# Kernel optimization log

Measured on AMD Instinct MI355X. Metric: run time of the kernel, lower is better.

The kernel has to match this reference:

```python
import jax, jax.numpy as jnp
import numpy as np

N_NODES = 50000
N_EDGES = 800000
N_GRAPHS = 64
D = 96              # input_dim = hidden_dim = output_dim
N_GIN = 4           # num_layers - 1 GINConv layers
N_HEADS = 5         # num_layers linear_prediction heads
BN_EPS = 1e-5


def setup_inputs() -> dict:
    key = jax.random.key(0)
    ks = jax.random.split(key, 16)
    s = 1.0 / np.sqrt(D)
    h = jax.random.normal(ks[0], (N_NODES, D), dtype=jnp.float32)
    src = jax.random.randint(ks[1], (N_EDGES,), 0, N_NODES, dtype=jnp.int32)
    dst = jax.random.randint(ks[2], (N_EDGES,), 0, N_NODES, dtype=jnp.int32)
    # sorted node->graph ids; deterministic so every graph is non-empty
    graph_ids = (jnp.arange(N_NODES, dtype=jnp.int32) * N_GRAPHS) // N_NODES
    return {
        "h": h,
        # GIN layer MLPs (num_mlp_layers=2): Linear -> BN -> ReLU -> Linear
        "gin_W1": jax.random.uniform(ks[3], (N_GIN, D, D), jnp.float32, -s, s),
        "gin_b1": jax.random.uniform(ks[4], (N_GIN, D), jnp.float32, -s, s),
        "gin_bn1_g": jnp.ones((N_GIN, D), jnp.float32),
        "gin_bn1_b": jnp.zeros((N_GIN, D), jnp.float32),
        "gin_W2": jax.random.uniform(ks[5], (N_GIN, D, D), jnp.float32, -s, s),
        "gin_b2": jax.random.uniform(ks[6], (N_GIN, D), jnp.float32, -s, s),
        # per-layer outer BatchNorm1d
        "bn_g": jnp.ones((N_GIN, D), jnp.float32),
        "bn_b": jnp.zeros((N_GIN, D), jnp.float32),
        # shared PReLU parameter (nn.PReLU default: 1 param, init 0.25)
        "prelu_a": jnp.full((1,), 0.25, jnp.float32),
        # linear_prediction heads
        "lin_W": jax.random.uniform(ks[7], (N_HEADS, D, D), jnp.float32, -s, s),
        "lin_b": jax.random.uniform(ks[8], (N_HEADS, D), jnp.float32, -s, s),
        "src": src,
        "dst": dst,
        "graph_ids": graph_ids,
    }


def _batchnorm(x, gamma, beta):
    # training-mode batch statistics over the node dim (biased variance, as torch)
    m = jnp.mean(x, axis=0)
    v = jnp.var(x, axis=0)
    return gamma * (x - m) * jax.lax.rsqrt(v + BN_EPS) + beta


def reference(h, gin_W1, gin_b1, gin_bn1_g, gin_bn1_b, gin_W2, gin_b2,
              bn_g, bn_b, prelu_a, lin_W, lin_b, src, dst, graph_ids):
    hidden_rep = [h]
    for l in range(N_GIN):
        # GINConv, sum aggregation, eps=0 (learn_eps=False): (1+eps)*h + sum_{j in N(i)} h_j
        agg = jax.ops.segment_sum(h[src], dst, num_segments=N_NODES)  # [N, D]
        z = h + agg
        # apply_func MLP: Linear -> BN -> ReLU -> Linear
        z = jax.nn.relu(_batchnorm(z @ gin_W1[l] + gin_b1[l], gin_bn1_g[l], gin_bn1_b[l]))
        z = z @ gin_W2[l] + gin_b2[l]
        # outer BatchNorm + PReLU
        z = _batchnorm(z, bn_g[l], bn_b[l])
        h = jnp.where(z >= 0, z, prelu_a * z)
        hidden_rep.append(h)
    # max graph pooling + per-layer linear heads (dropout = identity in eval)
    reps = []
    for l, hr in enumerate(hidden_rep):
        pooled = jax.ops.segment_max(hr, graph_ids, num_segments=N_GRAPHS)  # [B, D]
        reps.append(pooled @ lin_W[l] + lin_b[l])
    # layer_aggregation='cat': stack on dim=-1 then flatten -> [B, D * (N_GIN+1)]
    return jnp.stack(reps, axis=-1).reshape(N_GRAPHS, -1)
```

## Files before the change

kernel.cpp:

```cpp
#include <hip/hip_runtime.h>
#include <hip/hip_bf16.h>

#define N_NODES 50000
#define N_EDGES 800000
#define N_GRAPHS 64
#define D 96
#define N_GIN 4
#define BN_EPS 1e-5f
#define PCH 64
#define GEMM_GRID 782
#define LP 104
#define ELLCAP 64

#define P1_BLOCKS 256
#define EPB 3125
#define BSH 8
#define BNODES 256
#define NBUCK 196
#define SPITCH 33

typedef __bf16 bf16;
typedef __bf16 bf16x8 __attribute__((ext_vector_type(8)));
typedef float f32x4 __attribute__((ext_vector_type(4)));
typedef unsigned short u16;
typedef unsigned int u32;

__device__ inline unsigned enc(float f) {
    unsigned b = __float_as_uint(f);
    return (b & 0x80000000u) ? ~b : (b | 0x80000000u);
}
__device__ inline float dec(unsigned u) {
    return __uint_as_float((u & 0x80000000u) ? (u ^ 0x80000000u) : ~u);
}

__global__ void k_prolog(const float* __restrict__ h, bf16* __restrict__ hb,
                         const float* __restrict__ W1, const float* __restrict__ W2,
                         bf16* __restrict__ wf, float* __restrict__ stats,
                         unsigned* __restrict__ pooledu) {
    int b = blockIdx.x;
    int tid = threadIdx.x;
    if (b < 2344) {
        int e = (b * 256 + tid) * 8;
        if (e >= N_NODES * D) return;
        float4 v0 = *(const float4*)(h + e);
        float4 v1 = *(const float4*)(h + e + 4);
        bf16x8 o;
        o[0] = (bf16)v0.x; o[1] = (bf16)v0.y; o[2] = (bf16)v0.z; o[3] = (bf16)v0.w;
        o[4] = (bf16)v1.x; o[5] = (bf16)v1.y; o[6] = (bf16)v1.z; o[7] = (bf16)v1.w;
        *(bf16x8*)(hb + e) = o;
    } else if (b < 2352) {
        int mat = b - 2344;
        const float* src = (mat < 4) ? (W1 + mat * D * D) : (W2 + (mat - 4) * D * D);
        bf16* dst = wf + mat * D * D;
        for (int p = tid; p < D * D; p += 256) {
            int f = p >> 9;
            int r = p & 511;
            int lane = r >> 3;
            int j = r & 7;
            int q = lane >> 4;
            int m16 = lane & 15;
            int nt = f / 3, ks = f % 3;
            int k = ks * 32 + q * 8 + j;
            int n = nt * 16 + m16;
            dst[p] = (bf16)src[k * D + n];
        }
    } else {
        int t = (b - 2352) * 256 + tid;
        if (t < N_GIN * 2 * 2 * D) stats[t] = 0.0f;
        if (t < 5 * N_GRAPHS * D) pooledu[t] = 0u;
    }
}

__global__ void __launch_bounds__(256) k_part_pool(
        const int* __restrict__ src, const int* __restrict__ dst,
        u32* __restrict__ eo, u16* __restrict__ offs,
        const bf16* __restrict__ hb, unsigned* __restrict__ pooledu) {
    __shared__ u16 sdst[EPB + 3];
    __shared__ u16 ssrc[EPB + 3];
    __shared__ int hist[256];
    __shared__ int incl[256];
    int tid = threadIdx.x;
    if (blockIdx.x < P1_BLOCKS) {
        int e0 = blockIdx.x * EPB;
        hist[tid] = 0;
        __syncthreads();
        for (int i = tid; i < EPB; i += 256) {
            int d = dst[e0 + i];
            sdst[i] = (u16)d;
            ssrc[i] = (u16)src[e0 + i];
            atomicAdd(&hist[d >> BSH], 1);
        }
        __syncthreads();
        int v = hist[tid];
        incl[tid] = v;
        __syncthreads();
        for (int o = 1; o < 256; o <<= 1) {
            int t = (tid >= o) ? incl[tid - o] : 0;
            __syncthreads();
            incl[tid] += t;
            __syncthreads();
        }
        int ex = incl[tid] - v;
        if (tid <= NBUCK) offs[tid * P1_BLOCKS + blockIdx.x] = (u16)ex;
        hist[tid] = ex;
        __syncthreads();
        for (int i = tid; i < EPB; i += 256) {
            int d = sdst[i];
            int pos = atomicAdd(&hist[d >> BSH], 1);
            eo[e0 + pos] = ((u32)(d & (BNODES - 1)) << 16) | (u32)ssrc[i];
        }
    } else {
        int grp = (blockIdx.x - P1_BLOCKS) * 16 + (tid >> 4);
        int l = tid & 15;
        if (l >= 12) return;
        int g = grp / PCH, c = grp % PCH;
        int gs = (g * N_NODES + N_GRAPHS - 1) / N_GRAPHS;
        int ge = ((g + 1) * N_NODES + N_GRAPHS - 1) / N_GRAPHS;
        int len = ge - gs;
        int rs = gs + (len * c) / PCH;
        int re = gs + (len * (c + 1)) / PCH;
        const bf16x8* __restrict__ base = (const bf16x8*)hb;
        float m[8];
#pragma unroll
        for (int j = 0; j < 8; ++j) m[j] = -3e38f;
        int i = rs;
        for (; i + 2 <= re; i += 2) {
            bf16x8 r0 = base[i * 12 + l];
            bf16x8 r1 = base[(i + 1) * 12 + l];
#pragma unroll
            for (int j = 0; j < 8; ++j) m[j] = fmaxf(m[j], fmaxf((float)r0[j], (float)r1[j]));
        }
        if (i < re) {
            bf16x8 r = base[i * 12 + l];
#pragma unroll
            for (int j = 0; j < 8; ++j) m[j] = fmaxf(m[j], (float)r[j]);
        }
        unsigned* dstp = pooledu + (size_t)g * D + l * 8;
#pragma unroll
        for (int j = 0; j < 8; ++j) atomicMax(&dstp[j], enc(m[j]));
    }
}

__global__ void __launch_bounds__(256) k_ell_build(
        const u32* __restrict__ eo, const u16* __restrict__ offs,
        u16* __restrict__ ell, int* __restrict__ cnt) {
    __shared__ u32 sell32[BNODES * SPITCH];
    __shared__ int scnt[BNODES];
    int tid = threadIdx.x;
    int b = blockIdx.x;
    scnt[tid] = 0;
    __syncthreads();
    int beg = offs[b * P1_BLOCKS + tid];
    int end = offs[(b + 1) * P1_BLOCKS + tid];
    const u32* ep = eo + (size_t)tid * EPB;
    u16* srows = (u16*)sell32;
    for (int i = beg; i < end; ++i) {
        u32 pk = ep[i];
        int dl = pk >> 16;
        int pos = atomicAdd(&scnt[dl], 1);
        if (pos < ELLCAP) srows[dl * (2 * SPITCH) + pos] = (u16)pk;
    }
    __syncthreads();
    int node0 = b << BSH;
    int nn = min(BNODES, N_NODES - node0);
    if (tid < nn) cnt[node0 + tid] = scnt[tid];
    u32* gell = (u32*)(ell + (size_t)node0 * ELLCAP);
    for (int i = tid; i < nn * 32; i += 256) {
        gell[i] = sell32[(i >> 5) * SPITCH + (i & 31)];
    }
}

__global__ void __launch_bounds__(256) k_agg_gemm(
        const bf16* __restrict__ prev, const int* __restrict__ cnt,
        const u16* __restrict__ ell, const bf16* __restrict__ Bf,
        const float* __restrict__ bias, bf16* __restrict__ Z,
        float* __restrict__ ssum, float* __restrict__ sssq) {
    __shared__ bf16 sA[4][16 * LP];
    __shared__ float sr1[4][D], sr2[4][D];
    int tid = threadIdx.x;
    int lane = tid & 63, wv = tid >> 6;
    int q = lane >> 4, m16 = lane & 15;
    int strip = blockIdx.x * 4 + wv;

    float psum[6], pssq[6];
#pragma unroll
    for (int f = 0; f < 6; ++f) { psum[f] = 0.0f; pssq[f] = 0.0f; }

    if (strip < 3125) {
        const bf16x8* __restrict__ base = (const bf16x8*)prev;
        int grp = q, gl = m16;
#pragma unroll 1
        for (int r = 0; r < 4; ++r) {
            int node = strip * 16 + r * 4 + grp;
            if (gl < 12) {
                float acc[8];
                bf16x8 self = base[node * 12 + gl];
#pragma unroll
                for (int j = 0; j < 8; ++j) acc[j] = (float)self[j];
                int dg = cnt[node];
                if (dg > ELLCAP) dg = ELLCAP;
                const u16* ep = ell + (size_t)node * ELLCAP;
                int e = 0;
                for (; e + 8 <= dg; e += 8) {
                    int s0 = ep[e];
                    int s1 = ep[e + 1];
                    int s2 = ep[e + 2];
                    int s3 = ep[e + 3];
                    int s4 = ep[e + 4];
                    int s5 = ep[e + 5];
                    int s6 = ep[e + 6];
                    int s7 = ep[e + 7];
                    bf16x8 r0 = base[s0 * 12 + gl];
                    bf16x8 r1 = base[s1 * 12 + gl];
                    bf16x8 r2 = base[s2 * 12 + gl];
                    bf16x8 r3 = base[s3 * 12 + gl];
                    bf16x8 r4 = base[s4 * 12 + gl];
                    bf16x8 r5 = base[s5 * 12 + gl];
                    bf16x8 r6 = base[s6 * 12 + gl];
                    bf16x8 r7 = base[s7 * 12 + gl];
#pragma unroll
                    for (int j = 0; j < 8; ++j) {
                        acc[j] += (float)r0[j] + (float)r1[j] + (float)r2[j] + (float)r3[j]
                                + (float)r4[j] + (float)r5[j] + (float)r6[j] + (float)r7[j];
                    }
                }
                for (; e < dg; ++e) {
                    int s = ep[e];
                    bf16x8 rr = base[s * 12 + gl];
#pragma unroll
                    for (int j = 0; j < 8; ++j) acc[j] += (float)rr[j];
                }
                bf16x8 o;
#pragma unroll
                for (int j = 0; j < 8; ++j) o[j] = (bf16)acc[j];
                *(bf16x8*)&sA[wv][(r * 4 + grp) * LP + gl * 8] = o;
            }
        }
        __asm__ volatile("s_waitcnt lgkmcnt(0)" ::: "memory");

        bf16x8 bfr[18];
#pragma unroll
        for (int f = 0; f < 18; ++f) bfr[f] = *(const bf16x8*)(Bf + (f * 64 + lane) * 8);

        bf16x8 a0 = *(const bf16x8*)&sA[wv][m16 * LP + q * 8];
        bf16x8 a1 = *(const bf16x8*)&sA[wv][m16 * LP + 32 + q * 8];
        bf16x8 a2 = *(const bf16x8*)&sA[wv][m16 * LP + 64 + q * 8];

#pragma unroll
        for (int f = 0; f < 6; ++f) {
            f32x4 acc = {0.0f, 0.0f, 0.0f, 0.0f};
            acc = __builtin_amdgcn_mfma_f32_16x16x32_bf16(a0, bfr[f * 3 + 0], acc, 0, 0, 0);
            acc = __builtin_amdgcn_mfma_f32_16x16x32_bf16(a1, bfr[f * 3 + 1], acc, 0, 0, 0);
            acc = __builtin_amdgcn_mfma_f32_16x16x32_bf16(a2, bfr[f * 3 + 2], acc, 0, 0, 0);
            int col = f * 16 + m16;
            float bvf = bias[col];
            bf16* zp = Z + (size_t)(strip * 16 + q * 4) * D + col;
#pragma unroll
            for (int i = 0; i < 4; ++i) {
                float v = acc[i] + bvf;
                zp[(size_t)i * D] = (bf16)v;
                psum[f] += v;
                pssq[f] += v * v;
            }
        }
    }
#pragma unroll
    for (int f = 0; f < 6; ++f) {
        float r = psum[f];
        r += __shfl_xor(r, 16);
        r += __shfl_xor(r, 32);
        float r2 = pssq[f];
        r2 += __shfl_xor(r2, 16);
        r2 += __shfl_xor(r2, 32);
        if (lane < 16) {
            sr1[wv][f * 16 + lane] = r;
            sr2[wv][f * 16 + lane] = r2;
        }
    }
    __syncthreads();
    int t = wv * 64 + lane;
    if (t < D) {
        atomicAdd(&ssum[t], sr1[0][t] + sr1[1][t] + sr1[2][t] + sr1[3][t]);
    } else if (t < 2 * D) {
        int u = t - D;
        atomicAdd(&sssq[u], sr2[0][u] + sr2[1][u] + sr2[2][u] + sr2[3][u]);
    }
}

__global__ void k_transform(const bf16* __restrict__ Z, const float* __restrict__ st,
                            const float* __restrict__ gamma, const float* __restrict__ beta,
                            const float* __restrict__ pa, bf16* __restrict__ O) {
    __shared__ float cs[D], ct[D];
    int t = threadIdx.x;
    if (t < D) {
        float m = st[t] * (1.0f / N_NODES);
        float v = st[D + t] * (1.0f / N_NODES) - m * m;
        float inv = rsqrtf(v + BN_EPS);
        float sc = gamma[t] * inv;
        cs[t] = sc;
        ct[t] = beta[t] - m * sc;
    }
    __syncthreads();
    int e = (blockIdx.x * 256 + t) * 8;
    if (e >= N_NODES * D) return;
    float alpha = pa[0];
    int c = e % D;
    bf16x8 z = *(const bf16x8*)(Z + e);
    bf16x8 o;
#pragma unroll
    for (int j = 0; j < 8; ++j) {
        float v = (float)z[j] * cs[c + j] + ct[c + j];
        o[j] = (bf16)(v >= 0.0f ? v : alpha * v);
    }
    *(bf16x8*)(O + e) = o;
}

__global__ void __launch_bounds__(256) k_gemm_fused(
        const bf16* __restrict__ A, const bf16* __restrict__ Bf,
        const float* __restrict__ st, const float* __restrict__ gamma,
        const float* __restrict__ beta, const float* __restrict__ bias,
        bf16* __restrict__ Z, float* __restrict__ ssum, float* __restrict__ sssq,
        unsigned* __restrict__ poolu) {
    __shared__ float cs[D], ct[D];
    __shared__ float sr1[4][D];
    __shared__ float sr2[4][D];
    __shared__ unsigned pmax[2 * D];
    int tid = threadIdx.x;
    if (tid < D) {
        float m = st[tid] * (1.0f / N_NODES);
        float v = st[D + tid] * (1.0f / N_NODES) - m * m;
        float inv = rsqrtf(v + BN_EPS);
        float sc = gamma[tid] * inv;
        cs[tid] = sc;
        ct[tid] = beta[tid] - m * sc;
    }
    if (tid < 2 * D) pmax[tid] = 0u;
    __syncthreads();

    int lane = tid & 63;
    int wv = tid >> 6;
    int w = (blockIdx.x * blockDim.x + tid) >> 6;
    int nw = (gridDim.x * blockDim.x) >> 6;
    int q = lane >> 4, m16 = lane & 15;
    int g0 = (int)(((long long)blockIdx.x * 64) * N_GRAPHS / N_NODES);

    float as_[3][8], at_[3][8];
#pragma unroll
    for (int ks = 0; ks < 3; ++ks)
#pragma unroll
        for (int j = 0; j < 8; ++j) {
            as_[ks][j] = cs[ks * 32 + q * 8 + j];
            at_[ks][j] = ct[ks * 32 + q * 8 + j];
        }

    bf16x8 bfr[18];
#pragma unroll
    for (int f = 0; f < 18; ++f) bfr[f] = *(const bf16x8*)(Bf + (f * 64 + lane) * 8);
    float bv[6];
#pragma unroll
    for (int f = 0; f < 6; ++f) bv[f] = bias[f * 16 + m16];
    float psum[6], pssq[6];
#pragma unroll
    for (int f = 0; f < 6; ++f) { psum[f] = 0.0f; pssq[f] = 0.0f; }

    const int NSTRIP = N_NODES / 16;
    for (int s = w; s < NSTRIP; s += nw) {
        const bf16* arow = A + (size_t)(s * 16 + m16) * D;
        bf16x8 z0 = *(const bf16x8*)(arow + q * 8);
        bf16x8 z1 = *(const bf16x8*)(arow + 32 + q * 8);
        bf16x8 z2 = *(const bf16x8*)(arow + 64 + q * 8);
        bf16x8 a0, a1, a2;
#pragma unroll
        for (int j = 0; j < 8; ++j) {
            a0[j] = (bf16)fmaxf(0.0f, (float)z0[j] * as_[0][j] + at_[0][j]);
            a1[j] = (bf16)fmaxf(0.0f, (float)z1[j] * as_[1][j] + at_[1][j]);
            a2[j] = (bf16)fmaxf(0.0f, (float)z2[j] * as_[2][j] + at_[2][j]);
        }
#pragma unroll
        for (int f = 0; f < 6; ++f) {
            f32x4 acc = {0.0f, 0.0f, 0.0f, 0.0f};
            acc = __builtin_amdgcn_mfma_f32_16x16x32_bf16(a0, bfr[f * 3 + 0], acc, 0, 0, 0);
            acc = __builtin_amdgcn_mfma_f32_16x16x32_bf16(a1, bfr[f * 3 + 1], acc, 0, 0, 0);
            acc = __builtin_amdgcn_mfma_f32_16x16x32_bf16(a2, bfr[f * 3 + 2], acc, 0, 0, 0);
            int col = f * 16 + m16;
            bf16* zp = Z + (size_t)(s * 16 + q * 4) * D + col;
#pragma unroll
            for (int i = 0; i < 4; ++i) {
                float v = acc[i] + bv[f];
                zp[(size_t)i * D] = (bf16)v;
                psum[f] += v;
                pssq[f] += v * v;
                int row = s * 16 + q * 4 + i;
                int g = (int)(((unsigned)row * 64u) / 50000u);
                int slot = g - g0;
                if (slot >= 0 && slot < 2)
                    atomicMax(&pmax[slot * D + col], enc(v));
            }
        }
    }
#pragma unroll
    for (int f = 0; f < 6; ++f) {
        float r = psum[f];
        r += __shfl_xor(r, 16);
        r += __shfl_xor(r, 32);
        float r2 = pssq[f];
        r2 += __shfl_xor(r2, 16);
        r2 += __shfl_xor(r2, 32);
        if (lane < 16) {
            sr1[wv][f * 16 + lane] = r;
            sr2[wv][f * 16 + lane] = r2;
        }
    }
    __syncthreads();
    int t = wv * 64 + lane;
    if (t < D) {
        atomicAdd(&ssum[t], sr1[0][t] + sr1[1][t] + sr1[2][t] + sr1[3][t]);
    } else if (t < 2 * D) {
        int u = t - D;
        atomicAdd(&sssq[u], sr2[0][u] + sr2[1][u] + sr2[2][u] + sr2[3][u]);
    }
    if (t < 2 * D) {
        int sl = t / D, c = t % D;
        int gg = g0 + sl;
        if (gg < N_GRAPHS && pmax[t] != 0u)
            atomicMax(&poolu[gg * D + c], pmax[t]);
    }
}

__global__ void k_heads(const unsigned* __restrict__ pooledu, const float* __restrict__ stats,
                        const float* __restrict__ bng, const float* __restrict__ bnb,
                        const float* __restrict__ pa, const float* __restrict__ W,
                        const float* __restrict__ B, float* __restrict__ out) {
    __shared__ float pv[D];
    int b = blockIdx.x;
    int l = b >> 6;
    int g = b & 63;
    int d = threadIdx.x;
    if (d < D) {
        float m = dec(pooledu[(size_t)(l * N_GRAPHS + g) * D + d]);
        if (l > 0) {
            int gl = l - 1;
            const float* st = stats + (gl * 2 + 1) * 2 * D;
            float mean = st[d] * (1.0f / N_NODES);
            float var = st[D + d] * (1.0f / N_NODES) - mean * mean;
            float inv = rsqrtf(var + BN_EPS);
            float s = bng[gl * D + d] * inv;
            float t = bnb[gl * D + d] - mean * s;
            float v = m * s + t;
            m = (v >= 0.0f) ? v : pa[0] * v;
        }
        pv[d] = m;
    }
    __syncthreads();
    if (d >= D) return;
    const float* w = W + (size_t)l * D * D;
    float acc = B[l * D + d];
    for (int k = 0; k < D; ++k) acc += pv[k] * w[k * D + d];
    out[g * (5 * D) + d * 5 + l] = acc;
}

extern "C" void kernel_launch(void* const* d_in, const int* in_sizes, int n_in,
                              void* d_out, int out_size, void* d_ws, size_t ws_size,
                              hipStream_t stream) {
    const float* h     = (const float*)d_in[0];
    const float* gW1   = (const float*)d_in[1];
    const float* gb1   = (const float*)d_in[2];
    const float* bn1g  = (const float*)d_in[3];
    const float* bn1b  = (const float*)d_in[4];
    const float* gW2   = (const float*)d_in[5];
    const float* gb2   = (const float*)d_in[6];
    const float* bng   = (const float*)d_in[7];
    const float* bnb   = (const float*)d_in[8];
    const float* prelu = (const float*)d_in[9];
    const float* linW  = (const float*)d_in[10];
    const float* linb  = (const float*)d_in[11];
    const int*   srcv  = (const int*)d_in[12];
    const int*   dstv  = (const int*)d_in[13];
    float* out = (float*)d_out;

    char* base = (char*)d_ws;
    size_t off = 0;
    auto carve = [&](size_t bytes) -> void* {
        void* p = base + off;
        off += (bytes + 255) & ~(size_t)255;
        return p;
    };
    const size_t HB = (size_t)N_NODES * D;
    bf16* hb0   = (bf16*)carve(HB * 2);
    bf16* hb1   = (bf16*)carve(HB * 2);
    bf16* zb    = (bf16*)carve(HB * 2);
    bf16* ab    = (bf16*)carve(HB * 2);
    bf16* wf    = (bf16*)carve(8 * D * D * 2);
    float* stats = (float*)carve(N_GIN * 2 * 2 * D * 4);
    int* cnt    = (int*)carve((size_t)N_NODES * 4);
    u16* ell    = (u16*)carve((size_t)N_NODES * ELLCAP * 2);
    u32* eo     = (u32*)carve((size_t)N_EDGES * 4);
    u16* offs   = (u16*)carve((size_t)(NBUCK + 1) * P1_BLOCKS * 2);
    unsigned* pooledu = (unsigned*)carve(5 * N_GRAPHS * D * 4);

    k_prolog<<<2472, 256, 0, stream>>>(h, hb0, gW1, gW2, wf, stats, pooledu);
    k_part_pool<<<P1_BLOCKS + N_GRAPHS * PCH / 16, 256, 0, stream>>>(
        srcv, dstv, eo, offs, hb0, pooledu);
    k_ell_build<<<NBUCK, 256, 0, stream>>>(eo, offs, ell, cnt);

    const bf16* prev = hb0;
    for (int l = 0; l < N_GIN; ++l) {
        float* st1 = stats + (l * 2 + 0) * 2 * D;
        float* st2 = stats + (l * 2 + 1) * 2 * D;
        if (l > 0) {
            float* stp = stats + ((l - 1) * 2 + 1) * 2 * D;
            k_transform<<<2344, 256, 0, stream>>>(ab, stp, bng + (l - 1) * D,
                                                  bnb + (l - 1) * D, prelu, hb1);
            prev = hb1;
        }
        k_agg_gemm<<<GEMM_GRID, 256, 0, stream>>>(prev, cnt, ell, wf + l * D * D,
                                                  gb1 + l * D, zb, st1, st1 + D);
        k_gemm_fused<<<GEMM_GRID, 256, 0, stream>>>(zb, wf + (4 + l) * D * D, st1,
                                                    bn1g + l * D, bn1b + l * D,
                                                    gb2 + l * D, ab, st2, st2 + D,
                                                    pooledu + (size_t)(l + 1) * N_GRAPHS * D);
    }
    k_heads<<<5 * N_GRAPHS, 128, 0, stream>>>(pooledu, stats, bng, bnb, prelu,
                                              linW, linb, out);
}
```

Baseline: 458.0 us.

## Split aggregation strips across wave pairs and pad ELL rows with zero sentinel

Each 16-node strip in the aggregation+GEMM kernel is now handled by two waves instead of one: each wave gathers half the rows and computes half of the output columns, and the grid doubles. ELL rows are prefilled with a sentinel index pointing to an extra zero row appended to the feature buffers, so the neighbor loop rounds up to multiples of 8 and loads indices as one 16-byte vector with no scalar tail loop. This aims for more parallelism and memory-level concurrency in the latency-bound gather. The cost is extra zero-row loads, an added block barrier, and more atomic adds on the BN statistics from the larger grid.

```diff
diff --git a/kernel.cpp b/kernel.cpp
--- a/kernel.cpp
+++ b/kernel.cpp
@@ -9,8 +9,10 @@
 #define BN_EPS 1e-5f
 #define PCH 64
 #define GEMM_GRID 782
+#define AGG_GRID 1563
 #define LP 104
 #define ELLCAP 64
+#define SENT 50000
 
 #define P1_BLOCKS 256
 #define EPB 3125
@@ -24,6 +26,7 @@
 typedef float f32x4 __attribute__((ext_vector_type(4)));
 typedef unsigned short u16;
 typedef unsigned int u32;
+typedef unsigned short u16x8 __attribute__((ext_vector_type(8)));
 
 __device__ inline unsigned enc(float f) {
     unsigned b = __float_as_uint(f);
@@ -34,6 +37,7 @@
 }
 
 __global__ void k_prolog(const float* __restrict__ h, bf16* __restrict__ hb,
+                         bf16* __restrict__ hb1,
                          const float* __restrict__ W1, const float* __restrict__ W2,
                          bf16* __restrict__ wf, float* __restrict__ stats,
                          unsigned* __restrict__ pooledu) {
@@ -68,6 +72,10 @@
         int t = (b - 2352) * 256 + tid;
         if (t < N_GIN * 2 * 2 * D) stats[t] = 0.0f;
         if (t < 5 * N_GRAPHS * D) pooledu[t] = 0u;
+        if (t < D) {
+            hb[(size_t)SENT * D + t] = (bf16)0.0f;
+            hb1[(size_t)SENT * D + t] = (bf16)0.0f;
+        }
     }
 }
 
@@ -148,6 +156,7 @@
     __shared__ int scnt[BNODES];
     int tid = threadIdx.x;
     int b = blockIdx.x;
+    for (int i = tid; i < BNODES * SPITCH; i += 256) sell32[i] = 0xC350C350u;
     scnt[tid] = 0;
     __syncthreads();
     int beg = offs[b * P1_BLOCKS + tid];
@@ -175,23 +184,27 @@
         const u16* __restrict__ ell, const bf16* __restrict__ Bf,
         const float* __restrict__ bias, bf16* __restrict__ Z,
         float* __restrict__ ssum, float* __restrict__ sssq) {
-    __shared__ bf16 sA[4][16 * LP];
-    __shared__ float sr1[4][D], sr2[4][D];
+    __shared__ bf16 sA[2][16 * LP];
+    __shared__ float sr1[4][48], sr2[4][48];
     int tid = threadIdx.x;
     int lane = tid & 63, wv = tid >> 6;
     int q = lane >> 4, m16 = lane & 15;
-    int strip = blockIdx.x * 4 + wv;
-
-    float psum[6], pssq[6];
-#pragma unroll
-    for (int f = 0; f < 6; ++f) { psum[f] = 0.0f; pssq[f] = 0.0f; }
-
-    if (strip < 3125) {
+    int sidx = wv >> 1;
+    int half = wv & 1;
+    int strip = blockIdx.x * 2 + sidx;
+    bool valid = (strip < 3125);
+
+    float psum[3], pssq[3];
+#pragma unroll
+    for (int f3 = 0; f3 < 3; ++f3) { psum[f3] = 0.0f; pssq[f3] = 0.0f; }
+
+    if (valid) {
         const bf16x8* __restrict__ base = (const bf16x8*)prev;
-        int grp = q, gl = m16;
-#pragma unroll 1
-        for (int r = 0; r < 4; ++r) {
-            int node = strip * 16 + r * 4 + grp;
+        int gl = m16;
+#pragma unroll
+        for (int rr = 0; rr < 2; ++rr) {
+            int r = half * 2 + rr;
+            int node = strip * 16 + r * 4 + q;
             if (gl < 12) {
                 float acc[8];
                 bf16x8 self = base[node * 12 + gl];
@@ -199,91 +212,83 @@
                 for (int j = 0; j < 8; ++j) acc[j] = (float)self[j];
                 int dg = cnt[node];
                 if (dg > ELLCAP) dg = ELLCAP;
+                int dgr = (dg + 7) & ~7;
                 const u16* ep = ell + (size_t)node * ELLCAP;
-                int e = 0;
-                for (; e + 8 <= dg; e += 8) {
-                    int s0 = ep[e];
-                    int s1 = ep[e + 1];
-                    int s2 = ep[e + 2];
-                    int s3 = ep[e + 3];
-                    int s4 = ep[e + 4];
-                    int s5 = ep[e + 5];
-                    int s6 = ep[e + 6];
-                    int s7 = ep[e + 7];
-                    bf16x8 r0 = base[s0 * 12 + gl];
-                    bf16x8 r1 = base[s1 * 12 + gl];
-                    bf16x8 r2 = base[s2 * 12 + gl];
-                    bf16x8 r3 = base[s3 * 12 + gl];
-                    bf16x8 r4 = base[s4 * 12 + gl];
-                    bf16x8 r5 = base[s5 * 12 + gl];
-                    bf16x8 r6 = base[s6 * 12 + gl];
-                    bf16x8 r7 = base[s7 * 12 + gl];
+                for (int e = 0; e < dgr; e += 8) {
+                    u16x8 iv = *(const u16x8*)(ep + e);
+                    bf16x8 r0 = base[(int)iv[0] * 12 + gl];
+                    bf16x8 r1 = base[(int)iv[1] * 12 + gl];
+                    bf16x8 r2 = base[(int)iv[2] * 12 + gl];
+                    bf16x8 r3 = base[(int)iv[3] * 12 + gl];
+                    bf16x8 r4 = base[(int)iv[4] * 12 + gl];
+                    bf16x8 r5 = base[(int)iv[5] * 12 + gl];
+                    bf16x8 r6 = base[(int)iv[6] * 12 + gl];
+                    bf16x8 r7 = base[(int)iv[7] * 12 + gl];
 #pragma unroll
                     for (int j = 0; j < 8; ++j) {
                         acc[j] += (float)r0[j] + (float)r1[j] + (float)r2[j] + (float)r3[j]
                                 + (float)r4[j] + (float)r5[j] + (float)r6[j] + (float)r7[j];
                     }
                 }
-                for (; e < dg; ++e) {
-                    int s = ep[e];
-                    bf16x8 rr = base[s * 12 + gl];
-#pragma unroll
-                    for (int j = 0; j < 8; ++j) acc[j] += (float)rr[j];
-                }
                 bf16x8 o;
 #pragma unroll
                 for (int j = 0; j < 8; ++j) o[j] = (bf16)acc[j];
-                *(bf16x8*)&sA[wv][(r * 4 + grp) * LP + gl * 8] = o;
+                *(bf16x8*)&sA[sidx][(r * 4 + q) * LP + gl * 8] = o;
             }
         }
-        __asm__ volatile("s_waitcnt lgkmcnt(0)" ::: "memory");
-
-        bf16x8 bfr[18];
-#pragma unroll
-        for (int f = 0; f < 18; ++f) bfr[f] = *(const bf16x8*)(Bf + (f * 64 + lane) * 8);
-
-        bf16x8 a0 = *(const bf16x8*)&sA[wv][m16 * LP + q * 8];
-        bf16x8 a1 = *(const bf16x8*)&sA[wv][m16 * LP + 32 + q * 8];
-        bf16x8 a2 = *(const bf16x8*)&sA[wv][m16 * LP + 64 + q * 8];
-
-#pragma unroll
-        for (int f = 0; f < 6; ++f) {
+    }
+    __syncthreads();
+
+    if (valid) {
+        bf16x8 bfr[9];
+#pragma unroll
+        for (int j = 0; j < 9; ++j)
+            bfr[j] = *(const bf16x8*)(Bf + ((half * 9 + j) * 64 + lane) * 8);
+
+        bf16x8 a0 = *(const bf16x8*)&sA[sidx][m16 * LP + q * 8];
+        bf16x8 a1 = *(const bf16x8*)&sA[sidx][m16 * LP + 32 + q * 8];
+        bf16x8 a2 = *(const bf16x8*)&sA[sidx][m16 * LP + 64 + q * 8];
+
+#pragma unroll
+        for (int f3 = 0; f3 < 3; ++f3) {
             f32x4 acc = {0.0f, 0.0f, 0.0f, 0.0f};
-            acc = __builtin_amdgcn_mfma_f32_16x16x32_bf16(a0, bfr[f * 3 + 0], acc, 0, 0, 0);
-            acc = __builtin_amdgcn_mfma_f32_16x16x32_bf16(a1, bfr[f * 3 + 1], acc, 0, 0, 0);
-            acc = __builtin_amdgcn_mfma_f32_16x16x32_bf16(a2, bfr[f * 3 + 2], acc, 0, 0, 0);
-            int col = f * 16 + m16;
+            acc = __builtin_amdgcn_mfma_f32_16x16x32_bf16(a0, bfr[f3 * 3 + 0], acc, 0, 0, 0);
+            acc = __builtin_amdgcn_mfma_f32_16x16x32_bf16(a1, bfr[f3 * 3 + 1], acc, 0, 0, 0);
+            acc = __builtin_amdgcn_mfma_f32_16x16x32_bf16(a2, bfr[f3 * 3 + 2], acc, 0, 0, 0);
+            int col = (half * 3 + f3) * 16 + m16;
             float bvf = bias[col];
             bf16* zp = Z + (size_t)(strip * 16 + q * 4) * D + col;
 #pragma unroll
             for (int i = 0; i < 4; ++i) {
                 float v = acc[i] + bvf;
                 zp[(size_t)i * D] = (bf16)v;
-                psum[f] += v;
-                pssq[f] += v * v;
+                psum[f3] += v;
+                pssq[f3] += v * v;
             }
         }
     }
 #pragma unroll
-    for (int f = 0; f < 6; ++f) {
-        float r = psum[f];
+    for (int f3 = 0; f3 < 3; ++f3) {
+        float r = psum[f3];
         r += __shfl_xor(r, 16);
         r += __shfl_xor(r, 32);
-        float r2 = pssq[f];
+        float r2 = pssq[f3];
         r2 += __shfl_xor(r2, 16);
         r2 += __shfl_xor(r2, 32);
         if (lane < 16) {
-            sr1[wv][f * 16 + lane] = r;
-            sr2[wv][f * 16 + lane] = r2;
-        }
-    }
-    __syncthreads();
-    int t = wv * 64 + lane;
+            sr1[wv][f3 * 16 + lane] = r;
+            sr2[wv][f3 * 16 + lane] = r2;
+        }
+    }
+    __syncthreads();
+    int t = tid;
     if (t < D) {
-        atomicAdd(&ssum[t], sr1[0][t] + sr1[1][t] + sr1[2][t] + sr1[3][t]);
+        float v = (t < 48) ? sr1[0][t] + sr1[2][t] : sr1[1][t - 48] + sr1[3][t - 48];
+        atomicAdd(&ssum[t], v);
     } else if (t < 2 * D) {
         int u = t - D;
-        atomicAdd(&sssq[u], sr2[0][u] + sr2[1][u] + sr2[2][u] + sr2[3][u]);
+        float v = (u < 48) ? sr2[0][u] + sr2[2][u] : sr2[1][u - 48] + sr2[3][u - 48];
+        atomicAdd(&sssq[u], v);
     }
 }
 
@@ -486,8 +491,8 @@
         return p;
     };
     const size_t HB = (size_t)N_NODES * D;
-    bf16* hb0   = (bf16*)carve(HB * 2);
-    bf16* hb1   = (bf16*)carve(HB * 2);
+    bf16* hb0   = (bf16*)carve((HB + D) * 2);
+    bf16* hb1   = (bf16*)carve((HB + D) * 2);
     bf16* zb    = (bf16*)carve(HB * 2);
     bf16* ab    = (bf16*)carve(HB * 2);
     bf16* wf    = (bf16*)carve(8 * D * D * 2);
@@ -498,7 +503,7 @@
     u16* offs   = (u16*)carve((size_t)(NBUCK + 1) * P1_BLOCKS * 2);
     unsigned* pooledu = (unsigned*)carve(5 * N_GRAPHS * D * 4);
 
-    k_prolog<<<2472, 256, 0, stream>>>(h, hb0, gW1, gW2, wf, stats, pooledu);
+    k_prolog<<<2472, 256, 0, stream>>>(h, hb0, hb1, gW1, gW2, wf, stats, pooledu);
     k_part_pool<<<P1_BLOCKS + N_GRAPHS * PCH / 16, 256, 0, stream>>>(
         srcv, dstv, eo, offs, hb0, pooledu);
     k_ell_build<<<NBUCK, 256, 0, stream>>>(eo, offs, ell, cnt);
@@ -513,8 +518,8 @@
                                                   bnb + (l - 1) * D, prelu, hb1);
             prev = hb1;
         }
-        k_agg_gemm<<<GEMM_GRID, 256, 0, stream>>>(prev, cnt, ell, wf + l * D * D,
-                                                  gb1 + l * D, zb, st1, st1 + D);
+        k_agg_gemm<<<AGG_GRID, 256, 0, stream>>>(prev, cnt, ell, wf + l * D * D,
+                                                 gb1 + l * D, zb, st1, st1 + D);
         k_gemm_fused<<<GEMM_GRID, 256, 0, stream>>>(zb, wf + (4 + l) * D * D, st1,
                                                     bn1g + l * D, bn1b + l * D,
                                                     gb2 + l * D, ab, st2, st2 + D,
```

Measured after the change: 483.2 us. +5.5%, slower.

## Pad ELL rows with zero sentinel node and gather two nodes per iteration

Applied to the files above, without the earlier changes.

Fills ELL slots past each node's degree with a sentinel index that points at an extra zeroed row appended to the feature buffers. This removes the scalar tail loop and allows 16-byte vectorized index loads. Each lane now processes two nodes at once, which doubles the number of independent gathers in flight to hide memory latency. The cost is wasted gathers of the zero row up to the rounded maximum degree of each node pair, plus extra work to fill shared memory in the ELL build.

```diff
diff --git a/kernel.cpp b/kernel.cpp
--- a/kernel.cpp
+++ b/kernel.cpp
@@ -11,6 +11,7 @@
 #define GEMM_GRID 782
 #define LP 104
 #define ELLCAP 64
+#define SENT 50000
 
 #define P1_BLOCKS 256
 #define EPB 3125
@@ -24,6 +25,7 @@
 typedef float f32x4 __attribute__((ext_vector_type(4)));
 typedef unsigned short u16;
 typedef unsigned int u32;
+typedef unsigned short u16x8 __attribute__((ext_vector_type(8)));
 
 __device__ inline unsigned enc(float f) {
     unsigned b = __float_as_uint(f);
@@ -34,6 +36,7 @@
 }
 
 __global__ void k_prolog(const float* __restrict__ h, bf16* __restrict__ hb,
+                         bf16* __restrict__ hb1,
                          const float* __restrict__ W1, const float* __restrict__ W2,
                          bf16* __restrict__ wf, float* __restrict__ stats,
                          unsigned* __restrict__ pooledu) {
@@ -68,6 +71,10 @@
         int t = (b - 2352) * 256 + tid;
         if (t < N_GIN * 2 * 2 * D) stats[t] = 0.0f;
         if (t < 5 * N_GRAPHS * D) pooledu[t] = 0u;
+        if (t < D) {
+            hb[(size_t)SENT * D + t] = (bf16)0.0f;
+            hb1[(size_t)SENT * D + t] = (bf16)0.0f;
+        }
     }
 }
 
@@ -148,6 +155,7 @@
     __shared__ int scnt[BNODES];
     int tid = threadIdx.x;
     int b = blockIdx.x;
+    for (int i = tid; i < BNODES * SPITCH; i += 256) sell32[i] = 0xC350C350u;
     scnt[tid] = 0;
     __syncthreads();
     int beg = offs[b * P1_BLOCKS + tid];
@@ -188,52 +196,54 @@
 
     if (strip < 3125) {
         const bf16x8* __restrict__ base = (const bf16x8*)prev;
-        int grp = q, gl = m16;
+        int gl = m16;
+        if (gl < 12) {
 #pragma unroll 1
-        for (int r = 0; r < 4; ++r) {
-            int node = strip * 16 + r * 4 + grp;
-            if (gl < 12) {
-                float acc[8];
-                bf16x8 self = base[node * 12 + gl];
-#pragma unroll
-                for (int j = 0; j < 8; ++j) acc[j] = (float)self[j];
-                int dg = cnt[node];
-                if (dg > ELLCAP) dg = ELLCAP;
-                const u16* ep = ell + (size_t)node * ELLCAP;
-                int e = 0;
-                for (; e + 8 <= dg; e += 8) {
-                    int s0 = ep[e];
-                    int s1 = ep[e + 1];
-                    int s2 = ep[e + 2];
-                    int s3 = ep[e + 3];
-                    int s4 = ep[e + 4];
-                    int s5 = ep[e + 5];
-                    int s6 = ep[e + 6];
-                    int s7 = ep[e + 7];
-                    bf16x8 r0 = base[s0 * 12 + gl];
-                    bf16x8 r1 = base[s1 * 12 + gl];
-                    bf16x8 r2 = base[s2 * 12 + gl];
-                    bf16x8 r3 = base[s3 * 12 + gl];
-                    bf16x8 r4 = base[s4 * 12 + gl];
-                    bf16x8 r5 = base[s5 * 12 + gl];
-                    bf16x8 r6 = base[s6 * 12 + gl];
-                    bf16x8 r7 = base[s7 * 12 + gl];
+            for (int rp = 0; rp < 2; ++rp) {
+                int nA = strip * 16 + rp * 8 + q;
+                int nB = nA + 4;
+                float accA[8], accB[8];
+                bf16x8 selfA = base[nA * 12 + gl];
+                bf16x8 selfB = base[nB * 12 + gl];
+#pragma unroll
+                for (int j = 0; j < 8; ++j) { accA[j] = (float)selfA[j]; accB[j] = (float)selfB[j]; }
+                int dgA = cnt[nA]; if (dgA > ELLCAP) dgA = ELLCAP;
+                int dgB = cnt[nB]; if (dgB > ELLCAP) dgB = ELLCAP;
+                int dgr = (((dgA > dgB) ? dgA : dgB) + 7) & ~7;
+                const u16* epA = ell + (size_t)nA * ELLCAP;
+                const u16* epB = ell + (size_t)nB * ELLCAP;
+                for (int e = 0; e < dgr; e += 8) {
+                    u16x8 ivA = *(const u16x8*)(epA + e);
+                    u16x8 ivB = *(const u16x8*)(epB + e);
+                    bf16x8 a0 = base[(int)ivA[0] * 12 + gl];
+                    bf16x8 a1 = base[(int)ivA[1] * 12 + gl];
+                    bf16x8 a2 = base[(int)ivA[2] * 12 + gl];
+                    bf16x8 a3 = base[(int)ivA[3] * 12 + gl];
+                    bf16x8 a4 = base[(int)ivA[4] * 12 + gl];
+                    bf16x8 a5 = base[(int)ivA[5] * 12 + gl];
+                    bf16x8 a6 = base[(int)ivA[6] * 12 + gl];
+                    bf16x8 a7 = base[(int)ivA[7] * 12 + gl];
+                    bf16x8 b0 = base[(int)ivB[0] * 12 + gl];
+                    bf16x8 b1 = base[(int)ivB[1] * 12 + gl];
+                    bf16x8 b2 = base[(int)ivB[2] * 12 + gl];
+                    bf16x8 b3 = base[(int)ivB[3] * 12 + gl];
+                    bf16x8 b4 = base[(int)ivB[4] * 12 + gl];
+                    bf16x8 b5 = base[(int)ivB[5] * 12 + gl];
+                    bf16x8 b6 = base[(int)ivB[6] * 12 + gl];
+                    bf16x8 b7 = base[(int)ivB[7] * 12 + gl];
 #pragma unroll
                     for (int j = 0; j < 8; ++j) {
-                        acc[j] += (float)r0[j] + (float)r1[j] + (float)r2[j] + (float)r3[j]
-                                + (float)r4[j] + (float)r5[j] + (float)r6[j] + (float)r7[j];
+                        accA[j] += (float)a0[j] + (float)a1[j] + (float)a2[j] + (float)a3[j]
+                                 + (float)a4[j] + (float)a5[j] + (float)a6[j] + (float)a7[j];
+                        accB[j] += (float)b0[j] + (float)b1[j] + (float)b2[j] + (float)b3[j]
+                                 + (float)b4[j] + (float)b5[j] + (float)b6[j] + (float)b7[j];
                     }
                 }
-                for (; e < dg; ++e) {
-                    int s = ep[e];
-                    bf16x8 rr = base[s * 12 + gl];
-#pragma unroll
-                    for (int j = 0; j < 8; ++j) acc[j] += (float)rr[j];
-                }
-                bf16x8 o;
-#pragma unroll
-                for (int j = 0; j < 8; ++j) o[j] = (bf16)acc[j];
-                *(bf16x8*)&sA[wv][(r * 4 + grp) * LP + gl * 8] = o;
+                bf16x8 oA, oB;
+#pragma unroll
+                for (int j = 0; j < 8; ++j) { oA[j] = (bf16)accA[j]; oB[j] = (bf16)accB[j]; }
+                *(bf16x8*)&sA[wv][(rp * 8 + q) * LP + gl * 8] = oA;
+                *(bf16x8*)&sA[wv][(rp * 8 + 4 + q) * LP + gl * 8] = oB;
             }
         }
         __asm__ volatile("s_waitcnt lgkmcnt(0)" ::: "memory");
@@ -486,8 +496,8 @@
         return p;
     };
     const size_t HB = (size_t)N_NODES * D;
-    bf16* hb0   = (bf16*)carve(HB * 2);
-    bf16* hb1   = (bf16*)carve(HB * 2);
+    bf16* hb0   = (bf16*)carve((HB + D) * 2);
+    bf16* hb1   = (bf16*)carve((HB + D) * 2);
     bf16* zb    = (bf16*)carve(HB * 2);
     bf16* ab    = (bf16*)carve(HB * 2);
     bf16* wf    = (bf16*)carve(8 * D * D * 2);
@@ -498,7 +508,7 @@
     u16* offs   = (u16*)carve((size_t)(NBUCK + 1) * P1_BLOCKS * 2);
     unsigned* pooledu = (unsigned*)carve(5 * N_GRAPHS * D * 4);
 
-    k_prolog<<<2472, 256, 0, stream>>>(h, hb0, gW1, gW2, wf, stats, pooledu);
+    k_prolog<<<2472, 256, 0, stream>>>(h, hb0, hb1, gW1, gW2, wf, stats, pooledu);
     k_part_pool<<<P1_BLOCKS + N_GRAPHS * PCH / 16, 256, 0, stream>>>(
         srcv, dstv, eo, offs, hb0, pooledu);
     k_ell_build<<<NBUCK, 256, 0, stream>>>(eo, offs, ell, cnt);
```

Result: faster. 429.6 us (-6.2%).
